# Kernel optimization log

Measured on AMD Instinct MI355X. Metric: run time of the kernel, lower is better.

Reference implementation:

```python
import jax, jax.numpy as jnp
import numpy as np

D_LOGIC = 256
D_MEMORY = 256
NHEAD = 4
B, S = 2, 4096


def setup_inputs() -> dict:
    key = jax.random.key(0)
    ks = jax.random.split(key, 12)
    scale = 0.02
    x_logic = jax.random.normal(ks[0], (B, S, D_LOGIC), dtype=jnp.float32)
    x_memory = jax.random.normal(ks[1], (B, S, D_MEMORY), dtype=jnp.float32)
    mask = jax.random.randint(ks[2], (1, 1, S, S), 0, 2, dtype=jnp.int32)
    # torch nn.Linear weights are [out_features, in_features]
    Wq = jax.random.normal(ks[3], (D_LOGIC, D_LOGIC), dtype=jnp.float32) * scale
    bq = jnp.zeros((D_LOGIC,), dtype=jnp.float32)
    Wk = jax.random.normal(ks[4], (D_LOGIC, D_LOGIC), dtype=jnp.float32) * scale
    bk = jnp.zeros((D_LOGIC,), dtype=jnp.float32)
    Wv = jax.random.normal(ks[5], (D_MEMORY, D_MEMORY), dtype=jnp.float32) * scale
    bv = jnp.zeros((D_MEMORY,), dtype=jnp.float32)
    Wo = jax.random.normal(ks[6], (D_MEMORY, D_MEMORY), dtype=jnp.float32) * scale
    bo = jnp.zeros((D_MEMORY,), dtype=jnp.float32)
    return {"x_logic": x_logic, "x_memory": x_memory, "mask": mask,
            "Wq": Wq, "bq": bq, "Wk": Wk, "bk": bk,
            "Wv": Wv, "bv": bv, "Wo": Wo, "bo": bo}


def reference(x_logic, x_memory, mask, Wq, bq, Wk, bk, Wv, bv, Wo, bo):
    batch, seq, _ = x_logic.shape
    hd_l = D_LOGIC // NHEAD   # head_dim_logic
    hd_m = D_MEMORY // NHEAD  # head_dim_memory
    # Q, K from logic stream
    Q = (x_logic @ Wq.T + bq).reshape(batch, seq, NHEAD, hd_l)
    K = (x_logic @ Wk.T + bk).reshape(batch, seq, NHEAD, hd_l)
    # scores: [B, H, S, S]
    scores = jnp.einsum('bqhd,bkhd->bhqk', Q, K) / jnp.sqrt(jnp.float32(hd_l))
    scores = jnp.where(mask == 0, jnp.float32(-1e9), scores)
    attn = jax.nn.softmax(scores, axis=-1)
    # V from memory stream
    V = (x_memory @ Wv.T + bv).reshape(batch, seq, NHEAD, hd_m)
    out = jnp.einsum('bhqk,bkhd->bqhd', attn, V).reshape(batch, seq, D_MEMORY)
    return out @ Wo.T + bo
```

## Files before the change

kernel.cpp:

```cpp
#include <hip/hip_runtime.h>

#define S_  4096
#define HD_ 64
#define H_  4
#define B_  2
#define DM  256
#define NS  4
#define KSPAN (S_ / NS)
#define NITER (KSPAN / 64)

typedef __bf16 bf16x8 __attribute__((ext_vector_type(8)));
typedef __bf16 bf16x4 __attribute__((ext_vector_type(4)));
typedef float  f32x4  __attribute__((ext_vector_type(4)));
typedef unsigned long long u64;

__device__ __forceinline__ bf16x8 cvt8(const float* p) {
    float4 u0 = *reinterpret_cast<const float4*>(p);
    float4 u1 = *reinterpret_cast<const float4*>(p + 4);
    bf16x8 r = { (__bf16)u0.x, (__bf16)u0.y, (__bf16)u0.z, (__bf16)u0.w,
                 (__bf16)u1.x, (__bf16)u1.y, (__bf16)u1.z, (__bf16)u1.w };
    return r;
}

__global__ __launch_bounds__(256) void pack_kernel(const int* __restrict__ mask,
                                                   u64* __restrict__ packed,
                                                   const float* __restrict__ Wq,
                                                   const float* __restrict__ Wk,
                                                   const float* __restrict__ Wv,
                                                   const float* __restrict__ Wo,
                                                   __bf16* __restrict__ wqb,
                                                   __bf16* __restrict__ wkb,
                                                   __bf16* __restrict__ wvb,
                                                   __bf16* __restrict__ wob) {
    const int bid = blockIdx.x;
    if (bid < 1024) {
        const int gw   = bid * 4 + (threadIdx.x >> 6);
        const int lane = threadIdx.x & 63;
        const int r  = lane >> 4;
        const int ll = lane & 15;
#pragma unroll
        for (int sb = 0; sb < 4; ++sb) {
            int4 v[4];
#pragma unroll
            for (int j = 0; j < 4; ++j) {
                const int u   = gw + (sb * 4 + j) * 4096;
                const int kbb = u & 63;
                const int q0  = (u >> 6) * 4;
                v[j] = *reinterpret_cast<const int4*>(
                    mask + (size_t)(q0 + r) * S_ + kbb * 64 + ll * 4);
            }
#pragma unroll
            for (int j = 0; j < 4; ++j) {
                const int u   = gw + (sb * 4 + j) * 4096;
                const int kbb = u & 63;
                const int q0  = (u >> 6) * 4;
                const u64 b0 = __ballot(v[j].x != 0);
                const u64 b1 = __ballot(v[j].y != 0);
                const u64 b2 = __ballot(v[j].z != 0);
                const u64 b3 = __ballot(v[j].w != 0);
                if (ll == 0) {
                    const u64 word = ((b0 >> (16 * r)) & 0xFFFFull)
                                   | (((b1 >> (16 * r)) & 0xFFFFull) << 16)
                                   | (((b2 >> (16 * r)) & 0xFFFFull) << 32)
                                   | (((b3 >> (16 * r)) & 0xFFFFull) << 48);
                    packed[(size_t)kbb * S_ + q0 + r] = word;
                }
            }
        }
        return;
    }
    const int t = (bid - 1024) * 256 + threadIdx.x;
#pragma unroll
    for (int j = 0; j < 4; ++j) {
        const int idx = t + j * 16384;
        const int arr = idx >> 14, k = idx & 16383;
        const float* src = arr == 0 ? Wq : arr == 1 ? Wk : arr == 2 ? Wv : Wo;
        __bf16* dst      = arr == 0 ? wqb : arr == 1 ? wkb : arr == 2 ? wvb : wob;
        float4 v = reinterpret_cast<const float4*>(src)[k];
        bf16x4 o = { (__bf16)v.x, (__bf16)v.y, (__bf16)v.z, (__bf16)v.w };
        reinterpret_cast<bf16x4*>(dst)[k] = o;
    }
}

__global__ __launch_bounds__(256) void proj_qkv_kernel(const float* __restrict__ xl,
                                                       const float* __restrict__ xm,
                                                       const __bf16* __restrict__ wqb,
                                                       const __bf16* __restrict__ wkb,
                                                       const __bf16* __restrict__ wvb,
                                                       const float* __restrict__ bq,
                                                       const float* __restrict__ bk,
                                                       const float* __restrict__ bv,
                                                       __bf16* __restrict__ Qb,
                                                       __bf16* __restrict__ Kb,
                                                       __bf16* __restrict__ Vtb) {
    const int mode = blockIdx.z;
    const int ny   = blockIdx.y;
    const float*  X    = (mode == 2) ? xm : xl;
    const __bf16* W    = (mode == 0) ? wqb : (mode == 1) ? wkb : wvb;
    const float*  bias = (mode == 0) ? bq : (mode == 1) ? bk : bv;
    const float scale  = (mode == 0) ? 0.18033688011112042f : 1.0f;

    const int wid  = threadIdx.x >> 6;
    const int lane = threadIdx.x & 63;
    const int g = lane >> 4, c = lane & 15;
    const int m0 = blockIdx.x * 64 + wid * 16;
    const float* Xp = X + (size_t)m0 * DM;

    f32x4 acc[8];
#pragma unroll
    for (int i = 0; i < 8; ++i) acc[i] = (f32x4){0.f, 0.f, 0.f, 0.f};

#pragma unroll
    for (int kf = 0; kf < 8; ++kf) {
        bf16x8 a = cvt8(Xp + c * DM + kf * 32 + g * 8);
#pragma unroll
        for (int nt = 0; nt < 8; ++nt) {
            bf16x8 b = *reinterpret_cast<const bf16x8*>(
                W + (size_t)(ny * 128 + nt * 16 + c) * DM + kf * 32 + g * 8);
            acc[nt] = __builtin_amdgcn_mfma_f32_16x16x32_bf16(a, b, acc[nt], 0, 0, 0);
        }
    }

#pragma unroll
    for (int nt = 0; nt < 8; ++nt) {
        const int n = ny * 128 + nt * 16 + c;
        const float bs = bias[n];
        const int h = n >> 6, d = n & 63;
#pragma unroll
        for (int r = 0; r < 4; ++r) {
            const int m = m0 + g * 4 + r;
            const float v = (acc[nt][r] + bs) * scale;
            const int b_ = m >> 12, s = m & (S_ - 1);
            if (mode == 0)
                Qb[((size_t)(b_ * H_ + h) * S_ + s) * HD_ + d] = (__bf16)v;
            else if (mode == 1)
                Kb[((size_t)(b_ * H_ + h) * S_ + s) * HD_ + d] = (__bf16)v;
            else
                Vtb[((size_t)(b_ * H_ + h) * HD_ + d) * S_ + s] = (__bf16)v;
        }
    }
}

__global__ __launch_bounds__(256, 4) void attn_kernel(const __bf16* __restrict__ Q,
                                                      const __bf16* __restrict__ K,
                                                      const __bf16* __restrict__ Vt,
                                                      const u64* __restrict__ packed,
                                                      __bf16* __restrict__ Opart,
                                                      float* __restrict__ Lpart) {
    __shared__ __bf16 Kt[2][64][72];
    __shared__ __bf16 Vl[2][64][72];
    __shared__ __bf16 Pl[4][16][72];

    const int bh = blockIdx.x;
    const int sp = blockIdx.y;
    const int qt = blockIdx.z;
    const int tid  = threadIdx.x;
    const int wid  = tid >> 6;
    const int lane = tid & 63;
    const int g = lane >> 4, c = lane & 15;
    const int q0w = qt * 64 + wid * 16;

    const __bf16* Qp = Q + ((size_t)bh * S_ + q0w) * HD_;
    bf16x8 qb0 = *reinterpret_cast<const bf16x8*>(Qp + c * HD_ + g * 8);
    bf16x8 qb1 = *reinterpret_cast<const bf16x8*>(Qp + c * HD_ + 32 + g * 8);

    const __bf16* Kp = K  + (size_t)bh * S_ * HD_;
    const __bf16* Vp = Vt + (size_t)bh * HD_ * S_;

    const int srow = tid >> 2;
    const int sseg = (tid & 3) * 16;

    f32x4 o[4];
#pragma unroll
    for (int i = 0; i < 4; ++i) o[i] = (f32x4){0.f, 0.f, 0.f, 0.f};
    float rs = 0.f;

    const int k0 = sp * KSPAN;
    const __bf16* kptr = Kp + (size_t)(k0 + srow) * HD_ + sseg;
    const __bf16* vptr = Vp + (size_t)srow * S_ + k0 + sseg;

    {
        bf16x8 a0 = *reinterpret_cast<const bf16x8*>(kptr);
        bf16x8 a1 = *reinterpret_cast<const bf16x8*>(kptr + 8);
        bf16x8 b0 = *reinterpret_cast<const bf16x8*>(vptr);
        bf16x8 b1 = *reinterpret_cast<const bf16x8*>(vptr + 8);
        *reinterpret_cast<bf16x8*>(&Kt[0][srow][sseg])     = a0;
        *reinterpret_cast<bf16x8*>(&Kt[0][srow][sseg + 8]) = a1;
        *reinterpret_cast<bf16x8*>(&Vl[0][srow][sseg])     = b0;
        *reinterpret_cast<bf16x8*>(&Vl[0][srow][sseg + 8]) = b1;
    }
    kptr += (size_t)64 * HD_;
    vptr += 64;
    bf16x8 kr0 = *reinterpret_cast<const bf16x8*>(kptr);
    bf16x8 kr1 = *reinterpret_cast<const bf16x8*>(kptr + 8);
    bf16x8 vr0 = *reinterpret_cast<const bf16x8*>(vptr);
    bf16x8 vr1 = *reinterpret_cast<const bf16x8*>(vptr + 8);
    __syncthreads();

    for (int it = 0; it < NITER; ++it) {
        const int cur = it & 1;
        const int kb = k0 + it * 64;

        if (it + 1 < NITER) {
            *reinterpret_cast<bf16x8*>(&Kt[cur ^ 1][srow][sseg])     = kr0;
            *reinterpret_cast<bf16x8*>(&Kt[cur ^ 1][srow][sseg + 8]) = kr1;
            *reinterpret_cast<bf16x8*>(&Vl[cur ^ 1][srow][sseg])     = vr0;
            *reinterpret_cast<bf16x8*>(&Vl[cur ^ 1][srow][sseg + 8]) = vr1;
        }
        if (it + 2 < NITER) {
            kptr += (size_t)64 * HD_;
            vptr += 64;
            kr0 = *reinterpret_cast<const bf16x8*>(kptr);
            kr1 = *reinterpret_cast<const bf16x8*>(kptr + 8);
            vr0 = *reinterpret_cast<const bf16x8*>(vptr);
            vr1 = *reinterpret_cast<const bf16x8*>(vptr + 8);
        }

        const u64 mw = packed[(size_t)(kb >> 6) * S_ + q0w + c];
        const unsigned wlo = (unsigned)mw, whi = (unsigned)(mw >> 32);

        f32x4 st[4];
        __builtin_amdgcn_s_setprio(1);
#pragma unroll
        for (int nt = 0; nt < 4; ++nt) {
            bf16x8 ka0 = *reinterpret_cast<const bf16x8*>(&Kt[cur][nt * 16 + c][g * 8]);
            bf16x8 ka1 = *reinterpret_cast<const bf16x8*>(&Kt[cur][nt * 16 + c][32 + g * 8]);
            f32x4 z = (f32x4){0.f, 0.f, 0.f, 0.f};
            st[nt] = __builtin_amdgcn_mfma_f32_16x16x32_bf16(ka0, qb0, z, 0, 0, 0);
            st[nt] = __builtin_amdgcn_mfma_f32_16x16x32_bf16(ka1, qb1, st[nt], 0, 0, 0);
        }
        __builtin_amdgcn_s_setprio(0);

#pragma unroll
        for (int nt = 0; nt < 4; ++nt) {
            const unsigned sh = nt * 4 + g;
            float p0 = ((wlo >> sh) & 1u)        ? exp2f(st[nt][0]) : 0.f;
            float p1 = ((wlo >> (sh + 16)) & 1u) ? exp2f(st[nt][1]) : 0.f;
            float p2 = ((whi >> sh) & 1u)        ? exp2f(st[nt][2]) : 0.f;
            float p3 = ((whi >> (sh + 16)) & 1u) ? exp2f(st[nt][3]) : 0.f;
            rs += (p0 + p1) + (p2 + p3);
            bf16x4 pw = { (__bf16)p0, (__bf16)p1, (__bf16)p2, (__bf16)p3 };
            *reinterpret_cast<bf16x4*>(&Pl[wid][c][nt * 16 + g * 4]) = pw;
        }

        bf16x8 pa0 = *reinterpret_cast<const bf16x8*>(&Pl[wid][c][g * 8]);
        bf16x8 pa1 = *reinterpret_cast<const bf16x8*>(&Pl[wid][c][32 + g * 8]);

        __builtin_amdgcn_s_setprio(1);
#pragma unroll
        for (int nt = 0; nt < 4; ++nt) {
            bf16x8 vb0 = *reinterpret_cast<const bf16x8*>(&Vl[cur][nt * 16 + c][g * 8]);
            bf16x8 vb1 = *reinterpret_cast<const bf16x8*>(&Vl[cur][nt * 16 + c][32 + g * 8]);
            o[nt] = __builtin_amdgcn_mfma_f32_16x16x32_bf16(pa0, vb0, o[nt], 0, 0, 0);
            o[nt] = __builtin_amdgcn_mfma_f32_16x16x32_bf16(pa1, vb1, o[nt], 0, 0, 0);
        }
        __builtin_amdgcn_s_setprio(0);

        if (it + 1 < NITER) __syncthreads();
    }

    rs += __shfl_xor(rs, 16);
    rs += __shfl_xor(rs, 32);
    if (lane < 16)
        Lpart[(size_t)(bh * NS + sp) * S_ + q0w + c] = rs;

    const size_t obase = ((size_t)(bh * NS + sp) * S_ + q0w) * 64;
#pragma unroll
    for (int nt = 0; nt < 4; ++nt) {
#pragma unroll
        for (int r = 0; r < 4; ++r)
            Opart[obase + (size_t)(g * 4 + r) * 64 + nt * 16 + c] = (__bf16)o[nt][r];
    }
}

__global__ __launch_bounds__(256) void proj_o_kernel(const __bf16* __restrict__ Opart,
                                                     const float* __restrict__ Lpart,
                                                     const __bf16* __restrict__ wob,
                                                     const float* __restrict__ bo,
                                                     float* __restrict__ out) {
    const int ny   = blockIdx.y;
    const int wid  = threadIdx.x >> 6;
    const int lane = threadIdx.x & 63;
    const int g = lane >> 4, c = lane & 15;
    const int m0 = blockIdx.x * 64 + wid * 16;

    const int row = m0 + c;
    const int b_ = row >> 12, s = row & (S_ - 1);

    f32x4 acc[8];
#pragma unroll
    for (int i = 0; i < 8; ++i) acc[i] = (f32x4){0.f, 0.f, 0.f, 0.f};

#pragma unroll
    for (int kf = 0; kf < 8; ++kf) {
        const int dcol = kf * 32 + g * 8;
        const int h = dcol >> 6, dm = dcol & 63;
        const int bh = b_ * H_ + h;
        float l = 0.f;
        float sum[8] = {0.f, 0.f, 0.f, 0.f, 0.f, 0.f, 0.f, 0.f};
#pragma unroll
        for (int sp = 0; sp < NS; ++sp) {
            l += Lpart[(size_t)(bh * NS + sp) * S_ + s];
            const size_t base = ((size_t)(bh * NS + sp) * S_ + s) * 64 + dm;
            bf16x8 p = *reinterpret_cast<const bf16x8*>(Opart + base);
#pragma unroll
            for (int j = 0; j < 8; ++j) sum[j] += (float)p[j];
        }
        const float invl = 1.0f / l;
        bf16x8 a = { (__bf16)(sum[0] * invl), (__bf16)(sum[1] * invl),
                     (__bf16)(sum[2] * invl), (__bf16)(sum[3] * invl),
                     (__bf16)(sum[4] * invl), (__bf16)(sum[5] * invl),
                     (__bf16)(sum[6] * invl), (__bf16)(sum[7] * invl) };
#pragma unroll
        for (int nt = 0; nt < 8; ++nt) {
            bf16x8 b = *reinterpret_cast<const bf16x8*>(
                wob + (size_t)(ny * 128 + nt * 16 + c) * DM + kf * 32 + g * 8);
            acc[nt] = __builtin_amdgcn_mfma_f32_16x16x32_bf16(a, b, acc[nt], 0, 0, 0);
        }
    }

#pragma unroll
    for (int nt = 0; nt < 8; ++nt) {
        const int n = ny * 128 + nt * 16 + c;
        const float bs = bo[n];
#pragma unroll
        for (int r = 0; r < 4; ++r) {
            const int m = m0 + g * 4 + r;
            out[(size_t)m * DM + n] = acc[nt][r] + bs;
        }
    }
}

extern "C" void kernel_launch(void* const* d_in, const int* in_sizes, int n_in,
                              void* d_out, int out_size, void* d_ws, size_t ws_size,
                              hipStream_t stream) {
    const float* x_logic  = (const float*)d_in[0];
    const float* x_memory = (const float*)d_in[1];
    const int*   mask     = (const int*)d_in[2];
    const float* Wq = (const float*)d_in[3];
    const float* bq = (const float*)d_in[4];
    const float* Wk = (const float*)d_in[5];
    const float* bk = (const float*)d_in[6];
    const float* Wv = (const float*)d_in[7];
    const float* bv = (const float*)d_in[8];
    const float* Wo = (const float*)d_in[9];
    const float* bo = (const float*)d_in[10];
    float* out = (float*)d_out;

    char* ws = (char*)d_ws;
    size_t off = 0;
    auto alloc = [&](size_t bytes) { char* p = ws + off; off += (bytes + 255) & ~255ull; return p; };

    const size_t NX = (size_t)B_ * S_ * DM;
    u64*    packed = (u64*)alloc((size_t)S_ * (S_ / 64) * 8);
    __bf16* wqb = (__bf16*)alloc((size_t)DM * DM * 2);
    __bf16* wkb = (__bf16*)alloc((size_t)DM * DM * 2);
    __bf16* wvb = (__bf16*)alloc((size_t)DM * DM * 2);
    __bf16* wob = (__bf16*)alloc((size_t)DM * DM * 2);
    __bf16* Qb  = (__bf16*)alloc(NX * 2);
    __bf16* Kb  = (__bf16*)alloc(NX * 2);
    __bf16* Vtb = (__bf16*)alloc(NX * 2);
    __bf16* Opart = (__bf16*)alloc((size_t)B_ * H_ * NS * S_ * HD_ * 2);
    float*  Lpart = (float*)alloc((size_t)B_ * H_ * NS * S_ * 4);

    pack_kernel<<<1088, 256, 0, stream>>>(mask, packed, Wq, Wk, Wv, Wo, wqb, wkb, wvb, wob);
    proj_qkv_kernel<<<dim3(128, 2, 3), 256, 0, stream>>>(x_logic, x_memory, wqb, wkb, wvb,
                                                         bq, bk, bv, Qb, Kb, Vtb);
    attn_kernel<<<dim3(8, NS, 64), 256, 0, stream>>>(Qb, Kb, Vtb, packed, Opart, Lpart);
    proj_o_kernel<<<dim3(128, 2), 256, 0, stream>>>(Opart, Lpart, wob, bo, out);
}
```

Before: 144.8 us.

## Load K and V fragments directly from global memory, dropping LDS staging

Removes the double-buffered shared-memory staging of K and V tiles in the attention kernel. Each wave now reads its MFMA operands straight from global memory (relying on L1/L2 cache), which also removes the per-iteration block barrier and the setprio hints. This cuts LDS traffic and synchronisation, but every wave now fetches the same K/V data separately and loses the software prefetch, so the loop may stall on global-load latency.

```diff
diff --git a/kernel.cpp b/kernel.cpp
--- a/kernel.cpp
+++ b/kernel.cpp
@@ -147,8 +147,6 @@
                                                       const u64* __restrict__ packed,
                                                       __bf16* __restrict__ Opart,
                                                       float* __restrict__ Lpart) {
-    __shared__ __bf16 Kt[2][64][72];
-    __shared__ __bf16 Vl[2][64][72];
     __shared__ __bf16 Pl[4][16][72];
 
     const int bh = blockIdx.x;
@@ -167,69 +165,30 @@
     const __bf16* Kp = K  + (size_t)bh * S_ * HD_;
     const __bf16* Vp = Vt + (size_t)bh * HD_ * S_;
 
-    const int srow = tid >> 2;
-    const int sseg = (tid & 3) * 16;
-
     f32x4 o[4];
 #pragma unroll
     for (int i = 0; i < 4; ++i) o[i] = (f32x4){0.f, 0.f, 0.f, 0.f};
     float rs = 0.f;
 
     const int k0 = sp * KSPAN;
-    const __bf16* kptr = Kp + (size_t)(k0 + srow) * HD_ + sseg;
-    const __bf16* vptr = Vp + (size_t)srow * S_ + k0 + sseg;
-
-    {
-        bf16x8 a0 = *reinterpret_cast<const bf16x8*>(kptr);
-        bf16x8 a1 = *reinterpret_cast<const bf16x8*>(kptr + 8);
-        bf16x8 b0 = *reinterpret_cast<const bf16x8*>(vptr);
-        bf16x8 b1 = *reinterpret_cast<const bf16x8*>(vptr + 8);
-        *reinterpret_cast<bf16x8*>(&Kt[0][srow][sseg])     = a0;
-        *reinterpret_cast<bf16x8*>(&Kt[0][srow][sseg + 8]) = a1;
-        *reinterpret_cast<bf16x8*>(&Vl[0][srow][sseg])     = b0;
-        *reinterpret_cast<bf16x8*>(&Vl[0][srow][sseg + 8]) = b1;
-    }
-    kptr += (size_t)64 * HD_;
-    vptr += 64;
-    bf16x8 kr0 = *reinterpret_cast<const bf16x8*>(kptr);
-    bf16x8 kr1 = *reinterpret_cast<const bf16x8*>(kptr + 8);
-    bf16x8 vr0 = *reinterpret_cast<const bf16x8*>(vptr);
-    bf16x8 vr1 = *reinterpret_cast<const bf16x8*>(vptr + 8);
-    __syncthreads();
 
     for (int it = 0; it < NITER; ++it) {
-        const int cur = it & 1;
         const int kb = k0 + it * 64;
-
-        if (it + 1 < NITER) {
-            *reinterpret_cast<bf16x8*>(&Kt[cur ^ 1][srow][sseg])     = kr0;
-            *reinterpret_cast<bf16x8*>(&Kt[cur ^ 1][srow][sseg + 8]) = kr1;
-            *reinterpret_cast<bf16x8*>(&Vl[cur ^ 1][srow][sseg])     = vr0;
-            *reinterpret_cast<bf16x8*>(&Vl[cur ^ 1][srow][sseg + 8]) = vr1;
-        }
-        if (it + 2 < NITER) {
-            kptr += (size_t)64 * HD_;
-            vptr += 64;
-            kr0 = *reinterpret_cast<const bf16x8*>(kptr);
-            kr1 = *reinterpret_cast<const bf16x8*>(kptr + 8);
-            vr0 = *reinterpret_cast<const bf16x8*>(vptr);
-            vr1 = *reinterpret_cast<const bf16x8*>(vptr + 8);
-        }
 
         const u64 mw = packed[(size_t)(kb >> 6) * S_ + q0w + c];
         const unsigned wlo = (unsigned)mw, whi = (unsigned)(mw >> 32);
 
+        const __bf16* kt = Kp + (size_t)kb * HD_;
         f32x4 st[4];
-        __builtin_amdgcn_s_setprio(1);
 #pragma unroll
         for (int nt = 0; nt < 4; ++nt) {
-            bf16x8 ka0 = *reinterpret_cast<const bf16x8*>(&Kt[cur][nt * 16 + c][g * 8]);
-            bf16x8 ka1 = *reinterpret_cast<const bf16x8*>(&Kt[cur][nt * 16 + c][32 + g * 8]);
+            const __bf16* kr = kt + (size_t)(nt * 16 + c) * HD_ + g * 8;
+            bf16x8 ka0 = *reinterpret_cast<const bf16x8*>(kr);
+            bf16x8 ka1 = *reinterpret_cast<const bf16x8*>(kr + 32);
             f32x4 z = (f32x4){0.f, 0.f, 0.f, 0.f};
             st[nt] = __builtin_amdgcn_mfma_f32_16x16x32_bf16(ka0, qb0, z, 0, 0, 0);
             st[nt] = __builtin_amdgcn_mfma_f32_16x16x32_bf16(ka1, qb1, st[nt], 0, 0, 0);
         }
-        __builtin_amdgcn_s_setprio(0);
 
 #pragma unroll
         for (int nt = 0; nt < 4; ++nt) {
@@ -246,17 +205,14 @@
         bf16x8 pa0 = *reinterpret_cast<const bf16x8*>(&Pl[wid][c][g * 8]);
         bf16x8 pa1 = *reinterpret_cast<const bf16x8*>(&Pl[wid][c][32 + g * 8]);
 
-        __builtin_amdgcn_s_setprio(1);
 #pragma unroll
         for (int nt = 0; nt < 4; ++nt) {
-            bf16x8 vb0 = *reinterpret_cast<const bf16x8*>(&Vl[cur][nt * 16 + c][g * 8]);
-            bf16x8 vb1 = *reinterpret_cast<const bf16x8*>(&Vl[cur][nt * 16 + c][32 + g * 8]);
+            const __bf16* vr = Vp + (size_t)(nt * 16 + c) * S_ + kb + g * 8;
+            bf16x8 vb0 = *reinterpret_cast<const bf16x8*>(vr);
+            bf16x8 vb1 = *reinterpret_cast<const bf16x8*>(vr + 32);
             o[nt] = __builtin_amdgcn_mfma_f32_16x16x32_bf16(pa0, vb0, o[nt], 0, 0, 0);
             o[nt] = __builtin_amdgcn_mfma_f32_16x16x32_bf16(pa1, vb1, o[nt], 0, 0, 0);
         }
-        __builtin_amdgcn_s_setprio(0);
-
-        if (it + 1 < NITER) __syncthreads();
     }
 
     rs += __shfl_xor(rs, 16);
```

Result: slower. 304.7 us (+110.5%).
